# Kernel optimization log

Measured on AMD Instinct MI355X. Metric: run time of the kernel, lower is better.

Reference implementation:

```python
import jax, jax.numpy as jnp
import numpy as np

N_NODES = 100000
N_EDGES = 1600000
IN_FEATS = 64
H_FEATS = 64
NUM_CLASSES = 32


def _cgnn(h, e, src, dst, W, b, n_nodes):
    # message: m = h[src] * e  (e is [E,1], broadcasts over feature dim)
    m = h[src] * e  # [E, F]
    # segment mean over destination nodes (DGL fn.mean -> 0 for isolated nodes)
    s = jax.ops.segment_sum(m, dst, num_segments=n_nodes)  # [N, F]
    deg = jax.ops.segment_sum(jnp.ones((m.shape[0],), m.dtype), dst,
                              num_segments=n_nodes)  # [N]
    h_N = s / jnp.maximum(deg, 1.0)[:, None]
    h_total = jnp.concatenate([h, h_N], axis=1)  # [N, 2F]
    return h_total @ W + b


def setup_inputs() -> dict:
    key = jax.random.key(0)
    k = jax.random.split(key, 8)
    in_feat = jax.random.normal(k[0], (N_NODES, IN_FEATS), dtype=jnp.float32)
    edge_feat = jax.random.uniform(k[1], (N_EDGES, 1), dtype=jnp.float32)
    src = jax.random.randint(k[2], (N_EDGES,), 0, N_NODES)
    dst = jax.random.randint(k[3], (N_EDGES,), 0, N_NODES)
    # Linear(2*in_feats, h_feats) and Linear(2*h_feats, num_classes)
    s1 = 1.0 / np.sqrt(2 * IN_FEATS)
    s2 = 1.0 / np.sqrt(2 * H_FEATS)
    W1 = jax.random.uniform(k[4], (2 * IN_FEATS, H_FEATS), jnp.float32, -s1, s1)
    b1 = jax.random.uniform(k[5], (H_FEATS,), jnp.float32, -s1, s1)
    W2 = jax.random.uniform(k[6], (2 * H_FEATS, NUM_CLASSES), jnp.float32, -s2, s2)
    b2 = jax.random.uniform(k[7], (NUM_CLASSES,), jnp.float32, -s2, s2)
    return {"in_feat": in_feat, "edge_feat": edge_feat, "src": src,
            "dst": dst, "W1": W1, "b1": b1, "W2": W2, "b2": b2}


def reference(in_feat, edge_feat, src, dst, W1, b1, W2, b2):
    h = _cgnn(in_feat, edge_feat, src, dst, W1, b1, N_NODES)
    h = jax.nn.relu(h)
    h = _cgnn(h, edge_feat, src, dst, W2, b2, N_NODES)
    return h
```

## Files before the change

### kernel.cpp

```cpp
#include <hip/hip_runtime.h>
#include <hip/hip_bf16.h>


#define F 64
#define NBMAX 2048
#define EPT 8
#define TPB 1024
#define EPB (EPT * TPB)
#define PADBKT 1280

__global__ __launch_bounds__(256) void init_cursor_kernel(
    int* __restrict__ bcursor, int nb)
{
    const int i = blockIdx.x * 256 + threadIdx.x;
    if (i < nb) bcursor[i] = i * PADBKT;
}

__global__ __launch_bounds__(TPB) void multisplit_kernel(
    const int* __restrict__ src, const int* __restrict__ dst,
    const float* __restrict__ ef, int* __restrict__ bcursor,
    int2* __restrict__ brec, int n_edges, int nb)
{
    __shared__ int lcnt[NBMAX];
    __shared__ int lbase[NBMAX];
    const int tid = threadIdx.x;
    for (int i = tid; i < nb; i += TPB) lcnt[i] = 0;
    __syncthreads();

    const int e0 = blockIdx.x * EPB + tid;
    int d[EPT], rk[EPT];
#pragma unroll
    for (int k = 0; k < EPT; ++k) {
        const int e = e0 + k * TPB;
        const int dd = (e < n_edges) ? dst[e] : -1;
        d[k]  = dd;
        rk[k] = (dd >= 0) ? atomicAdd(&lcnt[dd >> 6], 1) : 0;
    }
    __syncthreads();
    for (int i = tid; i < nb; i += TPB) {
        const int c = lcnt[i];
        lbase[i] = c ? atomicAdd(&bcursor[i], c) : 0;
    }
    __syncthreads();
#pragma unroll
    for (int k = 0; k < EPT; ++k) {
        const int e = e0 + k * TPB;
        if (e < n_edges) {
            const int dd  = d[k];
            const int bkt = dd >> 6;
            const int pos = lbase[bkt] + rk[k];
            if (pos < (bkt + 1) * PADBKT)
                brec[pos] = make_int2(((dd & 63) << 20) | src[e],
                                      __float_as_int(ef[e]));
        }
    }
}

__global__ __launch_bounds__(256) void bucket_sort_kernel(
    int2* __restrict__ brec, const int* __restrict__ bcursor,
    int* __restrict__ off2, int* __restrict__ end2,
    float* __restrict__ invdeg, int n_nodes)
{
    __shared__ int2 stage[PADBKT];
    __shared__ int  lcnt[64];
    __shared__ int  lcur[64];

    const int b   = blockIdx.x;
    const int tid = threadIdx.x;
    const int w0  = b * PADBKT;
    int cnt = bcursor[b] - w0;
    if (cnt > PADBKT) cnt = PADBKT;

    if (tid < 64) lcnt[tid] = 0;
    __syncthreads();

    for (int i = tid; i < cnt; i += 256) {
        const int2 r = brec[w0 + i];
        stage[i] = r;
        atomicAdd(&lcnt[r.x >> 20], 1);
    }
    __syncthreads();

    if (tid < 64) {
        const int c = lcnt[tid];
        int v = c;
        for (int d = 1; d < 64; d <<= 1) {
            int t = __shfl_up(v, d, 64);
            if (tid >= d) v += t;
        }
        const int excl = v - c;
        lcur[tid] = excl;
        const int node = (b << 6) + tid;
        if (node < n_nodes) {
            off2[node]   = w0 + excl;
            end2[node]   = w0 + excl + c;
            invdeg[node] = 1.0f / fmaxf((float)c, 1.0f);
        }
    }
    __syncthreads();

    for (int i = tid; i < cnt; i += 256) {
        const int2 r   = stage[i];
        const int  pos = atomicAdd(&lcur[r.x >> 20], 1);
        brec[w0 + pos] = make_int2((r.x & 0xFFFFF) << 7, r.y);
    }
}

__device__ __forceinline__ unsigned bf16_rne(float f)
{
    unsigned u = __float_as_uint(f);
    return (u + 0x7FFFu + ((u >> 16) & 1u)) >> 16;
}

__global__ __launch_bounds__(256) void f32_to_bf16_kernel(
    const float* __restrict__ x, unsigned short* __restrict__ y, int n8)
{
    const int i = blockIdx.x * 256 + threadIdx.x;
    if (i >= n8) return;
    const float4 a = ((const float4*)x)[2 * i];
    const float4 b = ((const float4*)x)[2 * i + 1];
    uint4 o;
    o.x = bf16_rne(a.x) | (bf16_rne(a.y) << 16);
    o.y = bf16_rne(a.z) | (bf16_rne(a.w) << 16);
    o.z = bf16_rne(b.x) | (bf16_rne(b.y) << 16);
    o.w = bf16_rne(b.z) | (bf16_rne(b.w) << 16);
    ((uint4*)y)[i] = o;
}

__global__ __launch_bounds__(256) void agg_kernel(
    const unsigned short* __restrict__ hb, const int2* __restrict__ rec,
    const int* __restrict__ off, const int* __restrict__ end,
    const float* __restrict__ invdeg, float* __restrict__ s, int n_nodes)
{
    const int wid  = (blockIdx.x * 256 + threadIdx.x) >> 6;
    const int lane = threadIdx.x & 63;
    const int n    = lane >> 5;
    const int r    = lane & 31;
    const int g    = r >> 3;
    const int q    = r & 7;

    const int  node   = wid * 2 + n;
    const bool active = node < n_nodes;
    const int  e0 = active ? off[node] : 0;
    const int  e1 = active ? end[node] : 0;

    const char* __restrict__ hq = (const char*)hb + q * 16;

    float4 aA0 = make_float4(0.f, 0.f, 0.f, 0.f);
    float4 aA1 = make_float4(0.f, 0.f, 0.f, 0.f);
    float4 aB0 = make_float4(0.f, 0.f, 0.f, 0.f);
    float4 aB1 = make_float4(0.f, 0.f, 0.f, 0.f);

    for (int base = e0; base < e1; base += 8) {
        const int  eA = base + g;
        const int  eB = base + 4 + g;
        const bool vA = eA < e1;
        const bool vB = eB < e1;
        const int2 rA = rec[vA ? eA : e0];
        const int2 rB = rec[vB ? eB : e0];
        const float evA = vA ? __int_as_float(rA.y) : 0.f;
        const float evB = vB ? __int_as_float(rB.y) : 0.f;
        const uint4 xA = *(const uint4*)(hq + rA.x);
        const uint4 xB = *(const uint4*)(hq + rB.x);

        aA0.x = fmaf(__uint_as_float(xA.x << 16),         evA, aA0.x);
        aA0.y = fmaf(__uint_as_float(xA.x & 0xFFFF0000u), evA, aA0.y);
        aA0.z = fmaf(__uint_as_float(xA.y << 16),         evA, aA0.z);
        aA0.w = fmaf(__uint_as_float(xA.y & 0xFFFF0000u), evA, aA0.w);
        aA1.x = fmaf(__uint_as_float(xA.z << 16),         evA, aA1.x);
        aA1.y = fmaf(__uint_as_float(xA.z & 0xFFFF0000u), evA, aA1.y);
        aA1.z = fmaf(__uint_as_float(xA.w << 16),         evA, aA1.z);
        aA1.w = fmaf(__uint_as_float(xA.w & 0xFFFF0000u), evA, aA1.w);

        aB0.x = fmaf(__uint_as_float(xB.x << 16),         evB, aB0.x);
        aB0.y = fmaf(__uint_as_float(xB.x & 0xFFFF0000u), evB, aB0.y);
        aB0.z = fmaf(__uint_as_float(xB.y << 16),         evB, aB0.z);
        aB0.w = fmaf(__uint_as_float(xB.y & 0xFFFF0000u), evB, aB0.w);
        aB1.x = fmaf(__uint_as_float(xB.z << 16),         evB, aB1.x);
        aB1.y = fmaf(__uint_as_float(xB.z & 0xFFFF0000u), evB, aB1.y);
        aB1.z = fmaf(__uint_as_float(xB.w << 16),         evB, aB1.z);
        aB1.w = fmaf(__uint_as_float(xB.w & 0xFFFF0000u), evB, aB1.w);
    }

    float4 a0 = make_float4(aA0.x + aB0.x, aA0.y + aB0.y,
                            aA0.z + aB0.z, aA0.w + aB0.w);
    float4 a1 = make_float4(aA1.x + aB1.x, aA1.y + aB1.y,
                            aA1.z + aB1.z, aA1.w + aB1.w);

#pragma unroll
    for (int m = 8; m <= 16; m <<= 1) {
        a0.x += __shfl_xor(a0.x, m); a0.y += __shfl_xor(a0.y, m);
        a0.z += __shfl_xor(a0.z, m); a0.w += __shfl_xor(a0.w, m);
        a1.x += __shfl_xor(a1.x, m); a1.y += __shfl_xor(a1.y, m);
        a1.z += __shfl_xor(a1.z, m); a1.w += __shfl_xor(a1.w, m);
    }

    if (g == 0 && active) {
        const float id = invdeg[node];
        float* __restrict__ srow = s + (size_t)node * F + q * 8;
        *(float4*)srow = make_float4(a0.x * id, a0.y * id, a0.z * id, a0.w * id);
        *(float4*)(srow + 4) = make_float4(a1.x * id, a1.y * id, a1.z * id, a1.w * id);
    }
}

template <int OUT, bool RELU, bool IN_BF16, bool OUT_BF16>
__global__ __launch_bounds__(256) void linear_lds_kernel(
    const float* __restrict__ hin_f, const unsigned short* __restrict__ hin_b,
    const float* __restrict__ s,
    const float* __restrict__ W, const float* __restrict__ b,
    float* __restrict__ out, unsigned short* __restrict__ hb_out, int n_nodes)
{
    constexpr int JT  = OUT / 4;
    constexpr int STR = 132;
    __shared__ float xin[64 * STR];

    const int tid   = threadIdx.x;
    const int node0 = blockIdx.x * 64;

    if constexpr (IN_BF16) {
        for (int i = tid; i < 512; i += 256) {
            const int ln = i >> 3, c8 = i & 7;
            const int node = node0 + ln;
            uint4 v = make_uint4(0u, 0u, 0u, 0u);
            if (node < n_nodes)
                v = *(const uint4*)&hin_b[(size_t)node * F + c8 * 8];
            float4 lo = make_float4(__uint_as_float(v.x << 16),
                                    __uint_as_float(v.x & 0xFFFF0000u),
                                    __uint_as_float(v.y << 16),
                                    __uint_as_float(v.y & 0xFFFF0000u));
            float4 hi = make_float4(__uint_as_float(v.z << 16),
                                    __uint_as_float(v.z & 0xFFFF0000u),
                                    __uint_as_float(v.w << 16),
                                    __uint_as_float(v.w & 0xFFFF0000u));
            *(float4*)&xin[ln * STR + c8 * 8]     = lo;
            *(float4*)&xin[ln * STR + c8 * 8 + 4] = hi;
        }
    } else {
        for (int i = tid; i < 1024; i += 256) {
            const int ln = i >> 4, c4 = i & 15;
            const int node = node0 + ln;
            float4 v = make_float4(0.f, 0.f, 0.f, 0.f);
            if (node < n_nodes)
                v = *(const float4*)&hin_f[(size_t)node * F + c4 * 4];
            *(float4*)&xin[ln * STR + c4 * 4] = v;
        }
    }
    for (int i = tid; i < 1024; i += 256) {
        const int ln = i >> 4, c4 = i & 15;
        const int node = node0 + ln;
        float4 v = make_float4(0.f, 0.f, 0.f, 0.f);
        if (node < n_nodes) v = *(const float4*)&s[(size_t)node * F + c4 * 4];
        *(float4*)&xin[ln * STR + F + c4 * 4] = v;
    }
    __syncthreads();

    const int lane = tid & 63;
    const int j0   = __builtin_amdgcn_readfirstlane((tid >> 6) * JT);

    float acc[JT];
#pragma unroll
    for (int j = 0; j < JT; ++j) acc[j] = b[j0 + j];

    const float* __restrict__ xrow = &xin[lane * STR];
#pragma unroll 2
    for (int k4 = 0; k4 < 32; ++k4) {
        const float4 xv = *(const float4*)&xrow[k4 * 4];
#pragma unroll
        for (int kk = 0; kk < 4; ++kk) {
            const int   k  = k4 * 4 + kk;
            const float xk = ((const float*)&xv)[kk];
#pragma unroll
            for (int j = 0; j < JT; ++j)
                acc[j] = fmaf(xk, W[k * OUT + j0 + j], acc[j]);
        }
    }

    const int node = node0 + lane;
    if (node < n_nodes) {
#pragma unroll
        for (int j = 0; j < JT; ++j) {
            float v = acc[j];
            if (RELU) v = fmaxf(v, 0.f);
            acc[j] = v;
        }
        if constexpr (OUT_BF16) {
            unsigned* __restrict__ hw =
                (unsigned*)(hb_out + (size_t)node * OUT + j0);
#pragma unroll
            for (int j = 0; j < JT; j += 2)
                hw[j >> 1] = bf16_rne(acc[j]) | (bf16_rne(acc[j + 1]) << 16);
        } else {
#pragma unroll
            for (int j = 0; j < JT; ++j)
                out[(size_t)node * OUT + j0 + j] = acc[j];
        }
    }
}

extern "C" void kernel_launch(void* const* d_in, const int* in_sizes, int n_in,
                              void* d_out, int out_size, void* d_ws, size_t ws_size,
                              hipStream_t stream)
{
    const float* in_feat   = (const float*)d_in[0];
    const float* edge_feat = (const float*)d_in[1];
    const int*   src       = (const int*)d_in[2];
    const int*   dst       = (const int*)d_in[3];
    const float* W1        = (const float*)d_in[4];
    const float* b1        = (const float*)d_in[5];
    const float* W2        = (const float*)d_in[6];
    const float* b2        = (const float*)d_in[7];
    float*       out       = (float*)d_out;

    const int n_nodes = in_sizes[0] / F;
    const int n_edges = in_sizes[2];
    const int nb      = (n_nodes + 63) >> 6;

    const int S = 100352;
    int*   wsi     = (int*)d_ws;
    int*   bcursor = wsi;
    int*   off2    = wsi + 2048;
    int*   end2    = wsi + 2048 + S;
    float* invdeg  = (float*)(wsi + 2048 + 2 * S);
    int2*  brec    = (int2*)(wsi + 2048 + 3 * S);
    float* s       = (float*)(brec + (size_t)nb * PADBKT);
    unsigned short* hb = (unsigned short*)(s + (size_t)n_nodes * F);

    const int egrid = (n_edges + EPB - 1) / EPB;
    init_cursor_kernel<<<(nb + 255) / 256, 256, 0, stream>>>(bcursor, nb);
    multisplit_kernel<<<egrid, TPB, 0, stream>>>(src, dst, edge_feat,
                                                 bcursor, brec, n_edges, nb);
    bucket_sort_kernel<<<nb, 256, 0, stream>>>(brec, bcursor, off2, end2,
                                               invdeg, n_nodes);

    const int n8    = (n_nodes * F) >> 3;
    const int cgrid = (n8 + 255) / 256;
    const int agrid = (n_nodes + 7) / 8;
    const int lgrid = (n_nodes + 63) / 64;

    f32_to_bf16_kernel<<<cgrid, 256, 0, stream>>>(in_feat, hb, n8);
    agg_kernel<<<agrid, 256, 0, stream>>>(hb, brec, off2, end2, invdeg, s, n_nodes);
    linear_lds_kernel<64, true, false, true><<<lgrid, 256, 0, stream>>>(
        in_feat, nullptr, s, W1, b1, nullptr, hb, n_nodes);

    agg_kernel<<<agrid, 256, 0, stream>>>(hb, brec, off2, end2, invdeg, s, n_nodes);
    linear_lds_kernel<32, false, true, false><<<lgrid, 256, 0, stream>>>(
        nullptr, hb, s, W2, b2, out, nullptr, n_nodes);
}
```

Baseline: 168.1 us.

## Use 256-node superbuckets in the multisplit and bucket-sort CSR build

The edge multisplit now groups edges by 256-node superbuckets instead of 64-node buckets. This cuts the number of global cursor atomics and shared-memory counters per block from about 1600 to about 400. The bucket sort kernel grows to 512 threads with a two-level scan over 256 local counters, and the packed record now uses 17 bits for the source index. The trade-off is that with fixed per-bucket padding, a superbucket holding more than 4864 edges silently drops records, and the 17-bit source field caps node ids at 131072.

```diff
diff --git a/kernel.cpp b/kernel.cpp
--- a/kernel.cpp
+++ b/kernel.cpp
@@ -3,28 +3,30 @@
 
 
 #define F 64
-#define NBMAX 2048
 #define EPT 8
 #define TPB 1024
 #define EPB (EPT * TPB)
-#define PADBKT 1280
+#define SBSHIFT 8
+#define SBSZ 256
+#define NSBMAX 512
+#define PADSB 4864
 
 __global__ __launch_bounds__(256) void init_cursor_kernel(
-    int* __restrict__ bcursor, int nb)
+    int* __restrict__ bcursor, int nsb)
 {
     const int i = blockIdx.x * 256 + threadIdx.x;
-    if (i < nb) bcursor[i] = i * PADBKT;
+    if (i < nsb) bcursor[i] = i * PADSB;
 }
 
 __global__ __launch_bounds__(TPB) void multisplit_kernel(
     const int* __restrict__ src, const int* __restrict__ dst,
     const float* __restrict__ ef, int* __restrict__ bcursor,
-    int2* __restrict__ brec, int n_edges, int nb)
-{
-    __shared__ int lcnt[NBMAX];
-    __shared__ int lbase[NBMAX];
+    int2* __restrict__ brec, int n_edges, int nsb)
+{
+    __shared__ int lcnt[NSBMAX];
+    __shared__ int lbase[NSBMAX];
     const int tid = threadIdx.x;
-    for (int i = tid; i < nb; i += TPB) lcnt[i] = 0;
+    for (int i = tid; i < nsb; i += TPB) lcnt[i] = 0;
     __syncthreads();
 
     const int e0 = blockIdx.x * EPB + tid;
@@ -34,10 +36,10 @@
         const int e = e0 + k * TPB;
         const int dd = (e < n_edges) ? dst[e] : -1;
         d[k]  = dd;
-        rk[k] = (dd >= 0) ? atomicAdd(&lcnt[dd >> 6], 1) : 0;
-    }
-    __syncthreads();
-    for (int i = tid; i < nb; i += TPB) {
+        rk[k] = (dd >= 0) ? atomicAdd(&lcnt[dd >> SBSHIFT], 1) : 0;
+    }
+    __syncthreads();
+    for (int i = tid; i < nsb; i += TPB) {
         const int c = lcnt[i];
         lbase[i] = c ? atomicAdd(&bcursor[i], c) : 0;
     }
@@ -47,50 +49,62 @@
         const int e = e0 + k * TPB;
         if (e < n_edges) {
             const int dd  = d[k];
-            const int bkt = dd >> 6;
+            const int bkt = dd >> SBSHIFT;
             const int pos = lbase[bkt] + rk[k];
-            if (pos < (bkt + 1) * PADBKT)
-                brec[pos] = make_int2(((dd & 63) << 20) | src[e],
+            if (pos < (bkt + 1) * PADSB)
+                brec[pos] = make_int2(((dd & (SBSZ - 1)) << 17) | src[e],
                                       __float_as_int(ef[e]));
         }
     }
 }
 
-__global__ __launch_bounds__(256) void bucket_sort_kernel(
+__global__ __launch_bounds__(512) void bucket_sort_kernel(
     int2* __restrict__ brec, const int* __restrict__ bcursor,
     int* __restrict__ off2, int* __restrict__ end2,
     float* __restrict__ invdeg, int n_nodes)
 {
-    __shared__ int2 stage[PADBKT];
-    __shared__ int  lcnt[64];
-    __shared__ int  lcur[64];
+    __shared__ int2 stage[PADSB];
+    __shared__ int  lcnt[SBSZ];
+    __shared__ int  lcur[SBSZ];
+    __shared__ int  wsum[4];
 
     const int b   = blockIdx.x;
     const int tid = threadIdx.x;
-    const int w0  = b * PADBKT;
+    const int w0  = b * PADSB;
     int cnt = bcursor[b] - w0;
-    if (cnt > PADBKT) cnt = PADBKT;
-
-    if (tid < 64) lcnt[tid] = 0;
-    __syncthreads();
-
-    for (int i = tid; i < cnt; i += 256) {
+    if (cnt > PADSB) cnt = PADSB;
+
+    if (tid < SBSZ) lcnt[tid] = 0;
+    __syncthreads();
+
+    for (int i = tid; i < cnt; i += 512) {
         const int2 r = brec[w0 + i];
         stage[i] = r;
-        atomicAdd(&lcnt[r.x >> 20], 1);
-    }
-    __syncthreads();
-
-    if (tid < 64) {
-        const int c = lcnt[tid];
-        int v = c;
+        atomicAdd(&lcnt[r.x >> 17], 1);
+    }
+    __syncthreads();
+
+    int v = 0, c = 0;
+    if (tid < SBSZ) {
+        c = lcnt[tid];
+        v = c;
         for (int d = 1; d < 64; d <<= 1) {
             int t = __shfl_up(v, d, 64);
-            if (tid >= d) v += t;
-        }
-        const int excl = v - c;
+            if ((tid & 63) >= d) v += t;
+        }
+        if ((tid & 63) == 63) wsum[tid >> 6] = v;
+    }
+    __syncthreads();
+    if (tid == 0) {
+        int a = 0;
+#pragma unroll
+        for (int i = 0; i < 4; ++i) { int t = wsum[i]; wsum[i] = a; a += t; }
+    }
+    __syncthreads();
+    if (tid < SBSZ) {
+        const int excl = wsum[tid >> 6] + (v - c);
         lcur[tid] = excl;
-        const int node = (b << 6) + tid;
+        const int node = (b << SBSHIFT) + tid;
         if (node < n_nodes) {
             off2[node]   = w0 + excl;
             end2[node]   = w0 + excl + c;
@@ -99,10 +113,10 @@
     }
     __syncthreads();
 
-    for (int i = tid; i < cnt; i += 256) {
+    for (int i = tid; i < cnt; i += 512) {
         const int2 r   = stage[i];
-        const int  pos = atomicAdd(&lcur[r.x >> 20], 1);
-        brec[w0 + pos] = make_int2((r.x & 0xFFFFF) << 7, r.y);
+        const int  pos = atomicAdd(&lcur[r.x >> 17], 1);
+        brec[w0 + pos] = make_int2((r.x & 0x1FFFF) << 7, r.y);
     }
 }
 
@@ -313,24 +327,24 @@
 
     const int n_nodes = in_sizes[0] / F;
     const int n_edges = in_sizes[2];
-    const int nb      = (n_nodes + 63) >> 6;
+    const int nsb     = (n_nodes + SBSZ - 1) >> SBSHIFT;
 
     const int S = 100352;
     int*   wsi     = (int*)d_ws;
     int*   bcursor = wsi;
-    int*   off2    = wsi + 2048;
-    int*   end2    = wsi + 2048 + S;
-    float* invdeg  = (float*)(wsi + 2048 + 2 * S);
-    int2*  brec    = (int2*)(wsi + 2048 + 3 * S);
-    float* s       = (float*)(brec + (size_t)nb * PADBKT);
+    int*   off2    = wsi + 1024;
+    int*   end2    = wsi + 1024 + S;
+    float* invdeg  = (float*)(wsi + 1024 + 2 * S);
+    int2*  brec    = (int2*)(wsi + 1024 + 3 * S);
+    float* s       = (float*)(brec + (size_t)nsb * PADSB);
     unsigned short* hb = (unsigned short*)(s + (size_t)n_nodes * F);
 
     const int egrid = (n_edges + EPB - 1) / EPB;
-    init_cursor_kernel<<<(nb + 255) / 256, 256, 0, stream>>>(bcursor, nb);
+    init_cursor_kernel<<<(nsb + 255) / 256, 256, 0, stream>>>(bcursor, nsb);
     multisplit_kernel<<<egrid, TPB, 0, stream>>>(src, dst, edge_feat,
-                                                 bcursor, brec, n_edges, nb);
-    bucket_sort_kernel<<<nb, 256, 0, stream>>>(brec, bcursor, off2, end2,
-                                               invdeg, n_nodes);
+                                                 bcursor, brec, n_edges, nsb);
+    bucket_sort_kernel<<<nsb, 512, 0, stream>>>(brec, bcursor, off2, end2,
+                                                invdeg, n_nodes);
 
     const int n8    = (n_nodes * F) >> 3;
     const int cgrid = (n8 + 255) / 256;
```

Measured after the change: 167.0 us. Within noise of the previous version (-0.7%).
